# Optimization experiments

Measured on AMD Instinct MI355X. Metric: run time of the kernel, lower is better.

The kernel has to match this reference:

```python
import jax, jax.numpy as jnp
import numpy as np

N, L, D = 8192, 50, 64          # nodes, max history length, embed_dim
NUM_USERS = 100000
NUM_ITEMS = 100000
NUM_RATINGS = 5


def setup_inputs() -> dict:
    key = jax.random.key(0)
    ks = jax.random.split(key, 12)
    g = lambda k, shp, s=0.05: jax.random.normal(k, shp, jnp.float32) * s
    return {
        "nodes": jax.random.randint(ks[0], (N,), 0, NUM_USERS),
        "history_uv": jax.random.randint(ks[1], (N, L), 0, NUM_ITEMS),
        "history_r": jax.random.randint(ks[2], (N, L), 0, NUM_RATINGS),
        "hist_len": jax.random.randint(ks[3], (N,), 1, L + 1),  # ragged lengths in [1, L]
        # embedding tables (v2e / u2e / r2e)
        "v2e": g(ks[4], (NUM_ITEMS, D), 0.1),
        "u2e": g(ks[5], (NUM_USERS, D), 0.1),
        "r2e": g(ks[6], (NUM_RATINGS, D), 0.1),
        # w_r1: Dense(2D -> D), w_r2: Dense(D -> D)
        "W1": g(ks[7], (2 * D, D)), "b1": jnp.zeros((D,), jnp.float32),
        "W2": g(ks[8], (D, D)), "b2": jnp.zeros((D,), jnp.float32),
        # Attention MLP: Dense(2D->D), Dense(D->D), Dense(D->1)
        "A1": g(ks[9], (2 * D, D)), "ab1": jnp.zeros((D,), jnp.float32),
        "A2": g(ks[10], (D, D)), "ab2": jnp.zeros((D,), jnp.float32),
        "A3": g(ks[11], (D, 1)), "ab3": jnp.zeros((1,), jnp.float32),
    }


def reference(nodes, history_uv, history_r, hist_len, v2e, u2e, r2e,
              W1, b1, W2, b2, A1, ab1, A2, ab2, A3, ab3):
    # Vectorized form of the per-node Python loop: pad histories to L, mask.
    e_uv = v2e[history_uv]                       # [N,L,D] neighbor item embeds
    uv_rep = u2e[nodes]                          # [N,D]   self (user) embed
    e_r = r2e[history_r]                         # [N,L,D] rating embeds
    x = jnp.concatenate([e_uv, e_r], axis=-1)    # [N,L,2D]
    x = jax.nn.relu(x @ W1 + b1)                 # w_r1 + relu
    o = jax.nn.relu(x @ W2 + b2)                 # w_r2 + relu -> o_history [N,L,D]
    # attention: concat(o_history, repeated uv_rep) -> 2-layer relu MLP -> scalar
    a_in = jnp.concatenate(
        [o, jnp.broadcast_to(uv_rep[:, None, :], o.shape)], axis=-1)  # [N,L,2D]
    h = jax.nn.relu(a_in @ A1 + ab1)
    h = jax.nn.relu(h @ A2 + ab2)
    s = (h @ A3 + ab3)[..., 0]                   # [N,L] attention logits
    mask = jnp.arange(L)[None, :] < hist_len[:, None]
    att = jax.nn.softmax(jnp.where(mask, s, -1e9), axis=-1)  # softmax over history
    # att_history = o_history^T @ att_w, per node -> [N,D]
    return jnp.einsum('nl,nld->nd', att, o)
```

## Files before the change

kernel.cpp:

```cpp
#include <hip/hip_runtime.h>
#include <hip/hip_bf16.h>
#include <stdint.h>

typedef short bfx8 __attribute__((ext_vector_type(8)));
typedef float f32x4 __attribute__((ext_vector_type(4)));

#define MFMA16(a, b, c) __builtin_amdgcn_mfma_f32_16x16x32_bf16(a, b, c, 0, 0, 0)
#define STAGE_FENCE() __builtin_amdgcn_sched_barrier(0x77)
#define PIN_FENCE()   __builtin_amdgcn_sched_barrier(0x47)

#define OFF_W1 0
#define OFF_A1 16384
#define OFF_W2 32768
#define OFF_A2 40960
#define OFF_CB 49152
#define OFF_TB 50448
#define CBB_B1  0
#define CBB_B2  256
#define CBB_AB1 512
#define CBB_AB2 768
#define CBB_A3  1024

__device__ __forceinline__ uint32_t pk2(float a, float b) {
    __hip_bfloat162 h = __float22bfloat162_rn(make_float2(a, b));
    union { __hip_bfloat162 h; uint32_t u; } cv; cv.h = h; return cv.u;
}
__device__ __forceinline__ float bflo(uint32_t w) { return __uint_as_float(w << 16); }
__device__ __forceinline__ float bfhi(uint32_t w) { return __uint_as_float(w & 0xFFFF0000u); }

__device__ __forceinline__ bfx8 pack8(const float4 a, const float4 b) {
    union { bfx8 v; uint32_t u[4]; } r;
    r.u[0] = pk2(a.x, a.y); r.u[1] = pk2(a.z, a.w);
    r.u[2] = pk2(b.x, b.y); r.u[3] = pk2(b.z, b.w);
    return r.v;
}
__device__ __forceinline__ bfx8 packr(f32x4 a, f32x4 b) {
    union { bfx8 v; uint32_t u[4]; } r;
    r.u[0] = pk2(fmaxf(a[0], 0.f), fmaxf(a[1], 0.f));
    r.u[1] = pk2(fmaxf(a[2], 0.f), fmaxf(a[3], 0.f));
    r.u[2] = pk2(fmaxf(b[0], 0.f), fmaxf(b[1], 0.f));
    r.u[3] = pk2(fmaxf(b[2], 0.f), fmaxf(b[3], 0.f));
    return r.v;
}
__device__ __forceinline__ float4 ld4(const float* p) { return *(const float4*)p; }

__device__ __forceinline__ int mix4(int row) {
    return (row & 3) | (((row >> 4) & 1) << 2) | (((row >> 3) & 1) << 3);
}
__device__ __forceinline__ int mix3(int row) {
    return (row & 3) | (((row >> 3) & 1) << 2);
}
template <int CTRL>
__device__ __forceinline__ float dppadd(float x) {
    int y = __builtin_amdgcn_update_dpp(0, __float_as_int(x), CTRL, 0xF, 0xF, false);
    return x + __int_as_float(y);
}
__device__ __forceinline__ float rowsum16(float x) {
    x = dppadd<0xB1>(x);
    x = dppadd<0x4E>(x);
    x = dppadd<0x124>(x);
    x = dppadd<0x128>(x);
    return x;
}

__global__ __launch_bounds__(512, 1) void uvagg_mfma(
    const int* __restrict__ nodes, const int* __restrict__ huv,
    const int* __restrict__ hr, const int* __restrict__ hlen,
    const float* __restrict__ v2e, const float* __restrict__ u2e,
    const float* __restrict__ r2e,
    const float* __restrict__ W1, const float* __restrict__ b1,
    const float* __restrict__ W2, const float* __restrict__ b2,
    const float* __restrict__ A1, const float* __restrict__ ab1,
    const float* __restrict__ A2, const float* __restrict__ ab2,
    const float* __restrict__ A3, const float* __restrict__ ab3f,
    float* __restrict__ out, int N, int L, int nwaves)
{
    __shared__ __align__(16) uint8_t smem[51808];
    float* cbf = (float*)(smem + OFF_CB);

    const int tid = threadIdx.x;
    for (int i = tid; i < 4096; i += 512) {
        int kp = i >> 6, d = i & 63;
        int addr = d * 256 + ((((kp >> 2) ^ mix4(d)) & 15) << 4) + ((kp & 3) << 2);
        *(uint32_t*)(smem + OFF_A1 + addr) = pk2(A1[(2 * kp) * 64 + d], A1[(2 * kp + 1) * 64 + d]);
        if (i < 2048)
            *(uint32_t*)(smem + OFF_W1 + addr) = pk2(W1[(2 * kp) * 64 + d], W1[(2 * kp + 1) * 64 + d]);
    }
    for (int i = tid; i < 2048; i += 512) {
        int kp = i >> 6, d = i & 63;
        int addr = d * 128 + ((((kp >> 2) ^ mix3(d)) & 7) << 4) + ((kp & 3) << 2);
        *(uint32_t*)(smem + OFF_W2 + addr) = pk2(W2[(2 * kp) * 64 + d], W2[(2 * kp + 1) * 64 + d]);
        *(uint32_t*)(smem + OFF_A2 + addr) = pk2(A2[(2 * kp) * 64 + d], A2[(2 * kp + 1) * 64 + d]);
    }
    for (int i = tid; i < 321; i += 512) {
        if (i < 64)       cbf[i]   = b1[i];
        else if (i < 128) cbf[i]   = b2[i - 64];
        else if (i < 192) cbf[i]   = ab1[i - 128];
        else if (i < 256) cbf[i]   = ab2[i - 192];
        else if (i < 320) cbf[i]   = A3[i - 256];
        else              cbf[320] = ab3f[0];
    }
    for (int i = tid; i < 320; i += 512) {
        const int rr_ = i >> 6, d = i & 63;
        const float* wcol = W1 + 64 * 64 + d;
        const float* rrow = r2e + rr_ * 64;
        float a0 = b1[d], a1 = 0.f, a2 = 0.f, a3 = 0.f;
        #pragma unroll
        for (int k2 = 0; k2 < 64; k2 += 4) {
            a0 = fmaf(wcol[(k2 + 0) * 64], rrow[k2 + 0], a0);
            a1 = fmaf(wcol[(k2 + 1) * 64], rrow[k2 + 1], a1);
            a2 = fmaf(wcol[(k2 + 2) * 64], rrow[k2 + 2], a2);
            a3 = fmaf(wcol[(k2 + 3) * 64], rrow[k2 + 3], a3);
        }
        *(float*)(smem + OFF_TB + rr_ * 272 + d * 4) = (a0 + a1) + (a2 + a3);
    }
    __syncthreads();

    const int lane = tid & 63;
    const int wid  = tid >> 6;
    const int s    = lane & 15;
    const int g    = lane >> 4;
    const int r    = s & 3;
    const int q    = s >> 2;
    const int rs   = 8 * q + r;

    const int cx = ((q >> 1) | ((q & 1) << 1));
    const int base1 = rs * 256 + ((g ^ r) << 4) + (cx << 6);
    const int base2 = rs * 128 + ((g ^ r) << 4) + ((q & 1) << 6);
    const uint8_t* pw0 = smem + (base1 ^ (0 << 6));
    const uint8_t* pw1 = smem + (base1 ^ (1 << 6));
    const uint8_t* pw2 = smem + (base1 ^ (2 << 6));
    const uint8_t* pw3 = smem + (base1 ^ (3 << 6));
    const uint8_t* pq0 = smem + (base2 ^ (0 << 6));
    const uint8_t* pq1 = smem + (base2 ^ (1 << 6));
    const uint8_t* pcb = smem + OFF_CB + 32 * g;
    const uint8_t* ptb = smem + OFF_TB + 32 * g;
    const float ab3 = cbf[320];

    for (int node = blockIdx.x * 8 + wid; node < N; node += nwaves) {
        const int hl = __builtin_amdgcn_readfirstlane(min(hlen[node], L));
        const int un = __builtin_amdgcn_readfirstlane(nodes[node]);

        const float* ur = u2e + (size_t)un * 64;
        const bfx8 uf2 = pack8(ld4(ur + 8 * g),      ld4(ur + 8 * g + 4));
        const bfx8 uf3 = pack8(ld4(ur + 32 + 8 * g), ld4(ur + 36 + 8 * g));

        const int idxlane = min(lane, L - 1);
        const int iu_all = huv[(size_t)node * L + idxlane];
        const int ir_all = hr [(size_t)node * L + idxlane];

        f32x4 h1base[4];
        #pragma unroll
        for (int mt = 0; mt < 4; ++mt) {
            const int dof = 4 * (mt & 1) + 32 * (mt >> 1);
            h1base[mt] = *(const f32x4*)(pcb + CBB_AB1 + dof * 4);
            h1base[mt] = MFMA16(*(const bfx8*)(pw2 + OFF_A1 + dof * 256), uf2, h1base[mt]);
            h1base[mt] = MFMA16(*(const bfx8*)(pw3 + OFF_A1 + dof * 256), uf3, h1base[mt]);
        }

        float zacc = 0.0f;
        f32x4 accO[4];
        #pragma unroll
        for (int i = 0; i < 4; ++i) accO[i] = f32x4{0.f, 0.f, 0.f, 0.f};

        const int ntile = (hl + 15) >> 4;

        float4 qa0, qa1, qa2, qa3;
        int irs;
        {
            const int slot0 = min(s, hl - 1);
            const int iu = __shfl(iu_all, slot0, 64);
            irs = __shfl(ir_all, slot0, 64);
            const float* vr = v2e + (size_t)iu * 64;
            qa0 = ld4(vr + 8 * g);      qa1 = ld4(vr + 8 * g + 4);
            qa2 = ld4(vr + 32 + 8 * g); qa3 = ld4(vr + 36 + 8 * g);
        }

        for (int tt = 0; tt < ntile; ++tt) {
            const int gslot = tt * 16 + s;
            const bfx8 f0 = pack8(qa0, qa1);
            const bfx8 f1 = pack8(qa2, qa3);
            const uint8_t* ptbr = ptb + irs * 272;

            f32x4 ah[4];
            #pragma unroll
            for (int mt = 0; mt < 4; ++mt) {
                const int dof = 4 * (mt & 1) + 32 * (mt >> 1);
                ah[mt] = *(const f32x4*)(ptbr + dof * 4);
                ah[mt] = MFMA16(*(const bfx8*)(pw0 + OFF_W1 + dof * 256), f0, ah[mt]);
                ah[mt] = MFMA16(*(const bfx8*)(pw1 + OFF_W1 + dof * 256), f1, ah[mt]);
            }
            const bfx8 x1a = packr(ah[0], ah[1]);
            const bfx8 x1b = packr(ah[2], ah[3]);

            if (tt + 1 < ntile) {
                const int nslot = min(tt * 16 + 16 + s, hl - 1);
                const int niu = __shfl(iu_all, nslot, 64);
                irs = __shfl(ir_all, nslot, 64);
                const float* vr = v2e + (size_t)niu * 64;
                qa0 = ld4(vr + 8 * g);      qa1 = ld4(vr + 8 * g + 4);
                qa2 = ld4(vr + 32 + 8 * g); qa3 = ld4(vr + 36 + 8 * g);
            }
            PIN_FENCE();

            f32x4 ao[4];
            #pragma unroll
            for (int mt = 0; mt < 4; ++mt) {
                const int dof = 4 * (mt & 1) + 32 * (mt >> 1);
                ao[mt] = *(const f32x4*)(pcb + CBB_B2 + dof * 4);
                ao[mt] = MFMA16(*(const bfx8*)(pq0 + OFF_W2 + dof * 128), x1a, ao[mt]);
                ao[mt] = MFMA16(*(const bfx8*)(pq1 + OFF_W2 + dof * 128), x1b, ao[mt]);
            }
            const bfx8 oa = packr(ao[0], ao[1]);
            const bfx8 ob = packr(ao[2], ao[3]);
            STAGE_FENCE();

            f32x4 h[4];
            #pragma unroll
            for (int mt = 0; mt < 4; ++mt) {
                const int dof = 4 * (mt & 1) + 32 * (mt >> 1);
                h[mt] = h1base[mt];
                h[mt] = MFMA16(*(const bfx8*)(pw0 + OFF_A1 + dof * 256), oa, h[mt]);
                h[mt] = MFMA16(*(const bfx8*)(pw1 + OFF_A1 + dof * 256), ob, h[mt]);
            }
            const bfx8 h1a = packr(h[0], h[1]);
            const bfx8 h1b = packr(h[2], h[3]);
            STAGE_FENCE();

            float part = 0.0f;
            #pragma unroll
            for (int mt = 0; mt < 4; ++mt) {
                const int dof = 4 * (mt & 1) + 32 * (mt >> 1);
                f32x4 h2 = *(const f32x4*)(pcb + CBB_AB2 + dof * 4);
                h2 = MFMA16(*(const bfx8*)(pq0 + OFF_A2 + dof * 128), h1a, h2);
                h2 = MFMA16(*(const bfx8*)(pq1 + OFF_A2 + dof * 128), h1b, h2);
                const f32x4 aq = *(const f32x4*)(pcb + CBB_A3 + dof * 4);
                part = fmaf(fmaxf(h2[0], 0.f), aq[0], part);
                part = fmaf(fmaxf(h2[1], 0.f), aq[1], part);
                part = fmaf(fmaxf(h2[2], 0.f), aq[2], part);
                part = fmaf(fmaxf(h2[3], 0.f), aq[3], part);
            }
            STAGE_FENCE();
            float p2 = part + __shfl_xor(part, 16, 64);
            const float sl = p2 + __shfl_xor(p2, 32, 64) + ab3;
            const float p = (gslot < hl) ? __expf(sl) : 0.0f;
            zacc += p;
            union { bfx8 v; uint32_t u[4]; } ua, ub;
            ua.v = oa; ub.v = ob;
            #pragma unroll
            for (int j = 0; j < 2; ++j) {
                accO[0][2*j+0] = fmaf(p, bflo(ua.u[j]),     accO[0][2*j+0]);
                accO[0][2*j+1] = fmaf(p, bfhi(ua.u[j]),     accO[0][2*j+1]);
                accO[1][2*j+0] = fmaf(p, bflo(ua.u[2 + j]), accO[1][2*j+0]);
                accO[1][2*j+1] = fmaf(p, bfhi(ua.u[2 + j]), accO[1][2*j+1]);
                accO[2][2*j+0] = fmaf(p, bflo(ub.u[j]),     accO[2][2*j+0]);
                accO[2][2*j+1] = fmaf(p, bfhi(ub.u[j]),     accO[2][2*j+1]);
                accO[3][2*j+0] = fmaf(p, bflo(ub.u[2 + j]), accO[3][2*j+0]);
                accO[3][2*j+1] = fmaf(p, bfhi(ub.u[2 + j]), accO[3][2*j+1]);
            }
        }

        const float Z = rowsum16(zacc);
        #pragma unroll
        for (int mt = 0; mt < 4; ++mt)
            #pragma unroll
            for (int rr2 = 0; rr2 < 4; ++rr2)
                accO[mt][rr2] = rowsum16(accO[mt][rr2]);
        const float inv = 1.0f / Z;
        if (s == 0) {
            float* op = out + (size_t)node * 64;
            #pragma unroll
            for (int mt = 0; mt < 4; ++mt) {
                const int dof = 8 * g + 4 * (mt & 1) + 32 * (mt >> 1);
                *(float4*)(op + dof) = make_float4(accO[mt][0] * inv, accO[mt][1] * inv,
                                                   accO[mt][2] * inv, accO[mt][3] * inv);
            }
        }
    }
}

extern "C" void kernel_launch(void* const* d_in, const int* in_sizes, int n_in,
                              void* d_out, int out_size, void* d_ws, size_t ws_size,
                              hipStream_t stream) {
    const int*   nodes = (const int*)d_in[0];
    const int*   huv   = (const int*)d_in[1];
    const int*   hrr   = (const int*)d_in[2];
    const int*   hlen  = (const int*)d_in[3];
    const float* v2e   = (const float*)d_in[4];
    const float* u2e   = (const float*)d_in[5];
    const float* r2e   = (const float*)d_in[6];
    const float* W1    = (const float*)d_in[7];
    const float* b1    = (const float*)d_in[8];
    const float* W2    = (const float*)d_in[9];
    const float* b2    = (const float*)d_in[10];
    const float* A1    = (const float*)d_in[11];
    const float* ab1   = (const float*)d_in[12];
    const float* A2    = (const float*)d_in[13];
    const float* ab2   = (const float*)d_in[14];
    const float* A3    = (const float*)d_in[15];
    const float* ab3   = (const float*)d_in[16];
    float* out = (float*)d_out;

    const int N = in_sizes[0];
    const int L = in_sizes[1] / N;

    const int blocks = (N + 7) / 8;
    const int nwaves = blocks * 8;

    hipLaunchKernelGGL(uvagg_mfma, dim3(blocks), dim3(512), 0, stream,
                       nodes, huv, hrr, hlen, v2e, u2e, r2e,
                       W1, b1, W2, b2, A1, ab1, A2, ab2, A3, ab3,
                       out, N, L, nwaves);
}
```

Baseline: 46.41 us.

## Hoist MFMA weight fragments into registers and use persistent 256-thread blocks

Loads all W1/A1/W2/A2 bf16 weight fragments from LDS into registers once per wave, so the per-tile MFMA chain no longer re-reads them from shared memory. Block size drops to 256 threads (4 waves) with launch bounds allowing 2 blocks per CU, and the grid is capped at 512 persistent blocks that stride over nodes. This cuts LDS traffic in the inner loop but raises VGPR pressure by 64 registers per lane, and each of the fewer blocks repeats the prologue weight conversion.

```diff
diff --git a/kernel.cpp b/kernel.cpp
--- a/kernel.cpp
+++ b/kernel.cpp
@@ -63,7 +63,7 @@
     return x;
 }
 
-__global__ __launch_bounds__(512, 1) void uvagg_mfma(
+__global__ __launch_bounds__(256, 2) void uvagg_mfma(
     const int* __restrict__ nodes, const int* __restrict__ huv,
     const int* __restrict__ hr, const int* __restrict__ hlen,
     const float* __restrict__ v2e, const float* __restrict__ u2e,
@@ -79,20 +79,20 @@
     float* cbf = (float*)(smem + OFF_CB);
 
     const int tid = threadIdx.x;
-    for (int i = tid; i < 4096; i += 512) {
+    for (int i = tid; i < 4096; i += 256) {
         int kp = i >> 6, d = i & 63;
         int addr = d * 256 + ((((kp >> 2) ^ mix4(d)) & 15) << 4) + ((kp & 3) << 2);
         *(uint32_t*)(smem + OFF_A1 + addr) = pk2(A1[(2 * kp) * 64 + d], A1[(2 * kp + 1) * 64 + d]);
         if (i < 2048)
             *(uint32_t*)(smem + OFF_W1 + addr) = pk2(W1[(2 * kp) * 64 + d], W1[(2 * kp + 1) * 64 + d]);
     }
-    for (int i = tid; i < 2048; i += 512) {
+    for (int i = tid; i < 2048; i += 256) {
         int kp = i >> 6, d = i & 63;
         int addr = d * 128 + ((((kp >> 2) ^ mix3(d)) & 7) << 4) + ((kp & 3) << 2);
         *(uint32_t*)(smem + OFF_W2 + addr) = pk2(W2[(2 * kp) * 64 + d], W2[(2 * kp + 1) * 64 + d]);
         *(uint32_t*)(smem + OFF_A2 + addr) = pk2(A2[(2 * kp) * 64 + d], A2[(2 * kp + 1) * 64 + d]);
     }
-    for (int i = tid; i < 321; i += 512) {
+    for (int i = tid; i < 321; i += 256) {
         if (i < 64)       cbf[i]   = b1[i];
         else if (i < 128) cbf[i]   = b2[i - 64];
         else if (i < 192) cbf[i]   = ab1[i - 128];
@@ -100,7 +100,7 @@
         else if (i < 320) cbf[i]   = A3[i - 256];
         else              cbf[320] = ab3f[0];
     }
-    for (int i = tid; i < 320; i += 512) {
+    for (int i = tid; i < 320; i += 256) {
         const int rr_ = i >> 6, d = i & 63;
         const float* wcol = W1 + 64 * 64 + d;
         const float* rrow = r2e + rr_ * 64;
@@ -137,7 +137,21 @@
     const uint8_t* ptb = smem + OFF_TB + 32 * g;
     const float ab3 = cbf[320];
 
-    for (int node = blockIdx.x * 8 + wid; node < N; node += nwaves) {
+    bfx8 w1f[4][2], a1f[4][2], w2f[4][2], a2f[4][2];
+    #pragma unroll
+    for (int mt = 0; mt < 4; ++mt) {
+        const int dof = 4 * (mt & 1) + 32 * (mt >> 1);
+        w1f[mt][0] = *(const bfx8*)(pw0 + OFF_W1 + dof * 256);
+        w1f[mt][1] = *(const bfx8*)(pw1 + OFF_W1 + dof * 256);
+        a1f[mt][0] = *(const bfx8*)(pw0 + OFF_A1 + dof * 256);
+        a1f[mt][1] = *(const bfx8*)(pw1 + OFF_A1 + dof * 256);
+        w2f[mt][0] = *(const bfx8*)(pq0 + OFF_W2 + dof * 128);
+        w2f[mt][1] = *(const bfx8*)(pq1 + OFF_W2 + dof * 128);
+        a2f[mt][0] = *(const bfx8*)(pq0 + OFF_A2 + dof * 128);
+        a2f[mt][1] = *(const bfx8*)(pq1 + OFF_A2 + dof * 128);
+    }
+
+    for (int node = blockIdx.x * 4 + wid; node < N; node += nwaves) {
         const int hl = __builtin_amdgcn_readfirstlane(min(hlen[node], L));
         const int un = __builtin_amdgcn_readfirstlane(nodes[node]);
 
@@ -187,8 +201,8 @@
             for (int mt = 0; mt < 4; ++mt) {
                 const int dof = 4 * (mt & 1) + 32 * (mt >> 1);
                 ah[mt] = *(const f32x4*)(ptbr + dof * 4);
-                ah[mt] = MFMA16(*(const bfx8*)(pw0 + OFF_W1 + dof * 256), f0, ah[mt]);
-                ah[mt] = MFMA16(*(const bfx8*)(pw1 + OFF_W1 + dof * 256), f1, ah[mt]);
+                ah[mt] = MFMA16(w1f[mt][0], f0, ah[mt]);
+                ah[mt] = MFMA16(w1f[mt][1], f1, ah[mt]);
             }
             const bfx8 x1a = packr(ah[0], ah[1]);
             const bfx8 x1b = packr(ah[2], ah[3]);
@@ -208,8 +222,8 @@
             for (int mt = 0; mt < 4; ++mt) {
                 const int dof = 4 * (mt & 1) + 32 * (mt >> 1);
                 ao[mt] = *(const f32x4*)(pcb + CBB_B2 + dof * 4);
-                ao[mt] = MFMA16(*(const bfx8*)(pq0 + OFF_W2 + dof * 128), x1a, ao[mt]);
-                ao[mt] = MFMA16(*(const bfx8*)(pq1 + OFF_W2 + dof * 128), x1b, ao[mt]);
+                ao[mt] = MFMA16(w2f[mt][0], x1a, ao[mt]);
+                ao[mt] = MFMA16(w2f[mt][1], x1b, ao[mt]);
             }
             const bfx8 oa = packr(ao[0], ao[1]);
             const bfx8 ob = packr(ao[2], ao[3]);
@@ -218,10 +232,9 @@
             f32x4 h[4];
             #pragma unroll
             for (int mt = 0; mt < 4; ++mt) {
-                const int dof = 4 * (mt & 1) + 32 * (mt >> 1);
                 h[mt] = h1base[mt];
-                h[mt] = MFMA16(*(const bfx8*)(pw0 + OFF_A1 + dof * 256), oa, h[mt]);
-                h[mt] = MFMA16(*(const bfx8*)(pw1 + OFF_A1 + dof * 256), ob, h[mt]);
+                h[mt] = MFMA16(a1f[mt][0], oa, h[mt]);
+                h[mt] = MFMA16(a1f[mt][1], ob, h[mt]);
             }
             const bfx8 h1a = packr(h[0], h[1]);
             const bfx8 h1b = packr(h[2], h[3]);
@@ -232,8 +245,8 @@
             for (int mt = 0; mt < 4; ++mt) {
                 const int dof = 4 * (mt & 1) + 32 * (mt >> 1);
                 f32x4 h2 = *(const f32x4*)(pcb + CBB_AB2 + dof * 4);
-                h2 = MFMA16(*(const bfx8*)(pq0 + OFF_A2 + dof * 128), h1a, h2);
-                h2 = MFMA16(*(const bfx8*)(pq1 + OFF_A2 + dof * 128), h1b, h2);
+                h2 = MFMA16(a2f[mt][0], h1a, h2);
+                h2 = MFMA16(a2f[mt][1], h1b, h2);
                 const f32x4 aq = *(const f32x4*)(pcb + CBB_A3 + dof * 4);
                 part = fmaf(fmaxf(h2[0], 0.f), aq[0], part);
                 part = fmaf(fmaxf(h2[1], 0.f), aq[1], part);
@@ -304,10 +317,11 @@
     const int N = in_sizes[0];
     const int L = in_sizes[1] / N;
 
-    const int blocks = (N + 7) / 8;
-    const int nwaves = blocks * 8;
-
-    hipLaunchKernelGGL(uvagg_mfma, dim3(blocks), dim3(512), 0, stream,
+    int blocks = (N + 3) / 4;
+    if (blocks > 512) blocks = 512;
+    const int nwaves = blocks * 4;
+
+    hipLaunchKernelGGL(uvagg_mfma, dim3(blocks), dim3(256), 0, stream,
                        nodes, huv, hrr, hlen, v2e, u2e, r2e,
                        W1, b1, W2, b2, A1, ab1, A2, ab2, A3, ab3,
                        out, N, L, nwaves);
```

Measured after the change: 49.73 us. +7.1%, slower.
